# Optimization experiments

Measured on AMD Instinct MI355X. Metric: run time of the kernel, lower is better.

The kernel has to match this reference:

```python
import jax, jax.numpy as jnp
import numpy as np

B, T, C = 2, 2048, 1024
NH = 16
HD = C // NH

def setup_inputs() -> dict:
    key = jax.random.key(0)
    k1, k2, k3 = jax.random.split(key, 3)
    x = jax.random.normal(k1, (B, T, C), dtype=jnp.float32)
    w_attn = jax.random.normal(k2, (C, 3 * C), dtype=jnp.float32) * 0.02
    w_proj = jax.random.normal(k3, (C, C), dtype=jnp.float32) * 0.02
    return {"x": x, "w_attn": w_attn, "w_proj": w_proj}

def reference(x, w_attn, w_proj):
    b, t, c = x.shape
    qkv = x @ w_attn                                  # [B,T,3C]
    q, k, v = jnp.split(qkv, 3, axis=-1)
    # [B,NH,T,HD]
    q = q.reshape(b, t, NH, HD).transpose(0, 2, 1, 3)
    k = k.reshape(b, t, NH, HD).transpose(0, 2, 1, 3)
    v = v.reshape(b, t, NH, HD).transpose(0, 2, 1, 3)
    scale = 1.0 / np.sqrt(HD).astype(np.float32)
    att = jnp.einsum('bhqd,bhkd->bhqk', q, k) * scale  # [B,NH,T,T]
    causal = jnp.tril(jnp.ones((t, t), dtype=bool))
    att = jnp.where(causal[None, None], att, jnp.float32(-jnp.inf))
    att = jax.nn.softmax(att, axis=-1)
    y = jnp.einsum('bhqk,bhkd->bhqd', att, v)          # [B,NH,T,HD]
    y = y.transpose(0, 2, 1, 3).reshape(b, t, c)
    return y @ w_proj
```

## Files before the change

### kernel.cpp

```cpp
#include <hip/hip_runtime.h>
#include <hip/hip_bf16.h>

#define BB 2
#define TT 2048
#define CCH 1024
#define NHH 16
#define HDD 64
#define M_TOK (BB*TT)
#define N_QKV (3*CCH)

typedef __attribute__((ext_vector_type(8))) short bf16x8;
typedef __attribute__((ext_vector_type(4))) float f32x4;
typedef unsigned short u16;
typedef unsigned int u32;

__device__ __forceinline__ u16 f2bf(float f) {
    union { float f; u32 u; } v; v.f = f;
    u32 u = v.u;
    u32 r = (u + 0x7FFFu + ((u >> 16) & 1u)) >> 16;
    return (u16)r;
}

__device__ __forceinline__ u32 pk_bf16(float a, float b) {
    u32 ua = __float_as_uint(a) + 0x8000u;
    u32 ub = __float_as_uint(b) + 0x8000u;
    return __builtin_amdgcn_perm(ub, ua, 0x07060302u);
}

__device__ __forceinline__ void async_copy16(const void* g, void* l) {
    __builtin_amdgcn_global_load_lds((__attribute__((address_space(1))) void*)g,
                                     (__attribute__((address_space(3))) void*)l,
                                     16, 0, 0);
}


__global__ __launch_bounds__(256) void cast_bf16_kernel(
    const float* __restrict__ src, u16* __restrict__ dst, int n4) {
    int i = blockIdx.x * 256 + threadIdx.x;
    if (i < n4) {
        float4 f = ((const float4*)src)[i];
        ushort4 o;
        o.x = f2bf(f.x); o.y = f2bf(f.y); o.z = f2bf(f.z); o.w = f2bf(f.w);
        ((ushort4*)dst)[i] = o;
    }
}

__global__ __launch_bounds__(256) void transpose_bf16_kernel(
    const float* __restrict__ src, u16* __restrict__ dst, int R, int Cn,
    int scale_rows, float sc) {
    __shared__ float tile[32][33];
    int c0 = blockIdx.x * 32, r0 = blockIdx.y * 32;
    int tx = threadIdx.x, ty = threadIdx.y;
#pragma unroll
    for (int i = ty; i < 32; i += 8)
        tile[i][tx] = src[(size_t)(r0 + i) * Cn + c0 + tx];
    __syncthreads();
#pragma unroll
    for (int i = ty; i < 32; i += 8) {
        float v = tile[tx][i];
        if (c0 + i < scale_rows) v *= sc;
        dst[(size_t)(c0 + i) * R + r0 + tx] = f2bf(v);
    }
}


template<int SWAP, int NJ>
__device__ __forceinline__ void gemm_kloop64(
    const u16* __restrict__ A, const u16* __restrict__ Bt, int K,
    int m0, int n0, int t, u16* __restrict__ As, u16* __restrict__ Bs,
    f32x4 (&acc)[4][4])
{
    int lane = t & 63, w = t >> 6;
    int mw = (w >> 1) * 64, nw = (w & 1) * (NJ * 16);
    int mr = lane & 15, quad = lane >> 4;
    int lr = lane >> 3;
    int cswz = (lane & 7) ^ lr;

    const u16* gA[4]; u16* lA[4];
#pragma unroll
    for (int p = 0; p < 4; ++p) {
        int grp = w * 4 + p;
        gA[p] = A + (size_t)(m0 + grp * 8 + lr) * K + cswz * 8;
        lA[p] = As + ((size_t)grp * 64 + lane) * 8;
    }
    const u16* gB[4]; u16* lB[4];
#pragma unroll
    for (int p = 0; p < NJ; ++p) {
        int grp = w * NJ + p;
        gB[p] = Bt + (size_t)(n0 + grp * 8 + lr) * K + cswz * 8;
        lB[p] = Bs + ((size_t)grp * 64 + lane) * 8;
    }

    int swm = mr & 7;
    for (int k0 = 0; k0 < K; k0 += 64) {
#pragma unroll
        for (int p = 0; p < 4; ++p) async_copy16(gA[p] + k0, lA[p]);
#pragma unroll
        for (int p = 0; p < NJ; ++p) async_copy16(gB[p] + k0, lB[p]);
        __syncthreads();
#pragma unroll
        for (int kk = 0; kk < 2; ++kk) {
            bf16x8 af[4], bfr[4];
#pragma unroll
            for (int i = 0; i < 4; ++i) {
                int r = mw + i * 16 + mr;
                af[i] = *(const bf16x8*)&As[r * 64 + (((kk * 4 + quad) ^ swm) << 3)];
            }
#pragma unroll
            for (int j = 0; j < NJ; ++j) {
                int r = nw + j * 16 + mr;
                bfr[j] = *(const bf16x8*)&Bs[r * 64 + (((kk * 4 + quad) ^ swm) << 3)];
            }
#pragma unroll
            for (int i = 0; i < 4; ++i)
#pragma unroll
                for (int j = 0; j < NJ; ++j) {
                    if (SWAP)
                        acc[i][j] = __builtin_amdgcn_mfma_f32_16x16x32_bf16(bfr[j], af[i], acc[i][j], 0, 0, 0);
                    else
                        acc[i][j] = __builtin_amdgcn_mfma_f32_16x16x32_bf16(af[i], bfr[j], acc[i][j], 0, 0, 0);
                }
        }
        __syncthreads();
    }
}


#define QKV_NK 16
#define QKV_AS_HALF 16384
#define QKV_BS_HALF 12288
#define QKV_SMEM_BYTES ((2*QKV_AS_HALF + 2*QKV_BS_HALF) * 2)

__global__ __launch_bounds__(512, 1) void qkv_gemm_kernel(
    const u16* __restrict__ A, const u16* __restrict__ Bt,
    u16* __restrict__ Qo, u16* __restrict__ Ko, u16* __restrict__ Vto)
{
    extern __shared__ __align__(16) u16 smem[];
    u16* AsB = smem;
    u16* BsB = smem + 2 * QKV_AS_HALF;
    int t = threadIdx.x;
    int lane = t & 63, w = t >> 6;
    int m0 = blockIdx.y * 256, n0 = blockIdx.x * 192;
    int mw = (w >> 1) * 64, nw = (w & 1) * 96;
    int mr = lane & 15, quad = lane >> 4, swm = mr & 7;

    f32x4 zero = {0.f, 0.f, 0.f, 0.f};
    f32x4 acc[4][6];
#pragma unroll
    for (int i = 0; i < 4; ++i)
#pragma unroll
        for (int j = 0; j < 6; ++j) acc[i][j] = zero;

    int lr = lane >> 3;
    int cswz = (lane & 7) ^ lr;
    const u16* gA[4]; int lAo[4];
#pragma unroll
    for (int p = 0; p < 4; ++p) {
        int grp = w * 4 + p;
        gA[p] = A + (size_t)(m0 + grp * 8 + lr) * CCH + cswz * 8;
        lAo[p] = (grp * 64 + lane) * 8;
    }
    const u16* gB[3]; int lBo[3];
#pragma unroll
    for (int p = 0; p < 3; ++p) {
        int grp = w * 3 + p;
        gB[p] = Bt + (size_t)(n0 + grp * 8 + lr) * CCH + cswz * 8;
        lBo[p] = (grp * 64 + lane) * 8;
    }

#define QKV_STAGE(K0, BUF) do {                                               \
    u16* dA_ = AsB + (BUF) * QKV_AS_HALF;                                     \
    u16* dB_ = BsB + (BUF) * QKV_BS_HALF;                                     \
    _Pragma("unroll") for (int p_ = 0; p_ < 4; ++p_)                          \
        async_copy16(gA[p_] + (K0), dA_ + lAo[p_]);                           \
    _Pragma("unroll") for (int p_ = 0; p_ < 3; ++p_)                          \
        async_copy16(gB[p_] + (K0), dB_ + lBo[p_]);                           \
  } while (0)

    QKV_STAGE(0, 0);
    QKV_STAGE(64, 1);

    for (int k = 0; k < QKV_NK; ++k) {
        int cur = k & 1;
        if (k == QKV_NK - 1) asm volatile("s_waitcnt vmcnt(0)" ::: "memory");
        else                 asm volatile("s_waitcnt vmcnt(7)" ::: "memory");
        __builtin_amdgcn_s_barrier();
        asm volatile("" ::: "memory");
        const u16* Ac = AsB + cur * QKV_AS_HALF;
        const u16* Bc = BsB + cur * QKV_BS_HALF;
        bf16x8 a0[4], a1[4], b0[6], b1[6];
#pragma unroll
        for (int i = 0; i < 4; ++i) {
            int r = (mw + i * 16 + mr) * 64;
            a0[i] = *(const bf16x8*)&Ac[r + ((quad ^ swm) << 3)];
            a1[i] = *(const bf16x8*)&Ac[r + (((quad + 4) ^ swm) << 3)];
        }
#pragma unroll
        for (int j = 0; j < 6; ++j) {
            int r = (nw + j * 16 + mr) * 64;
            b0[j] = *(const bf16x8*)&Bc[r + ((quad ^ swm) << 3)];
            b1[j] = *(const bf16x8*)&Bc[r + (((quad + 4) ^ swm) << 3)];
        }
#pragma unroll
        for (int i = 0; i < 4; ++i)
#pragma unroll
            for (int j = 0; j < 6; ++j)
                acc[i][j] = __builtin_amdgcn_mfma_f32_16x16x32_bf16(b0[j], a0[i], acc[i][j], 0, 0, 0);
        asm volatile("s_waitcnt lgkmcnt(0)" ::: "memory");
        __builtin_amdgcn_sched_barrier(0);
        __builtin_amdgcn_s_barrier();
        asm volatile("" ::: "memory");
        if (k < QKV_NK - 2) QKV_STAGE((k + 2) * 64, cur);
#pragma unroll
        for (int i = 0; i < 4; ++i)
#pragma unroll
            for (int j = 0; j < 6; ++j)
                acc[i][j] = __builtin_amdgcn_mfma_f32_16x16x32_bf16(b1[j], a1[i], acc[i][j], 0, 0, 0);
    }
#undef QKV_STAGE

#pragma unroll
    for (int i = 0; i < 4; ++i)
#pragma unroll
        for (int j = 0; j < 6; ++j) {
            int tok = m0 + mw + i * 16 + mr;
            int cg0 = n0 + nw + j * 16 + quad * 4;
            int part = cg0 >> 10;
            int cc = cg0 & 1023;
            int h = cc >> 6, d0 = cc & 63;
            int b = tok >> 11, tt = tok & 2047;
            int bh = b * NHH + h;
            if (part < 2) {
                u16* dstp = part ? Ko : Qo;
                uint2 o;
                o.x = pk_bf16(acc[i][j][0], acc[i][j][1]);
                o.y = pk_bf16(acc[i][j][2], acc[i][j][3]);
                *(uint2*)&dstp[((size_t)bh * TT + tt) * HDD + d0] = o;
            } else {
#pragma unroll
                for (int r = 0; r < 4; ++r)
                    Vto[((size_t)bh * HDD + d0 + r) * TT + tt] = f2bf(acc[i][j][r]);
            }
        }
}


__global__ __launch_bounds__(256) void proj_gemm_kernel(
    const u16* __restrict__ A, const u16* __restrict__ Bt, float* __restrict__ Cout)
{
    __shared__ u16 As[128 * 64];
    __shared__ u16 Bs[64 * 64];
    int t = threadIdx.x;
    int m0 = blockIdx.y * 128, n0 = blockIdx.x * 64;
    int lane = t & 63, w = t >> 6;
    int mw = (w >> 1) * 64, nw = (w & 1) * 32;
    int mr = lane & 15, quad = lane >> 4;

    f32x4 zero = {0.f, 0.f, 0.f, 0.f};
    f32x4 acc[4][4];
#pragma unroll
    for (int i = 0; i < 4; ++i)
#pragma unroll
        for (int j = 0; j < 4; ++j) acc[i][j] = zero;

    gemm_kloop64<1, 2>(A, Bt, CCH, m0, n0, t, As, Bs, acc);

#pragma unroll
    for (int i = 0; i < 4; ++i)
#pragma unroll
        for (int j = 0; j < 2; ++j) {
            int tok = m0 + mw + i * 16 + mr;
            int cg0 = n0 + nw + j * 16 + quad * 4;
            float4 v;
            v.x = acc[i][j][0]; v.y = acc[i][j][1];
            v.z = acc[i][j][2]; v.w = acc[i][j][3];
            *(float4*)&Cout[(size_t)tok * CCH + cg0] = v;
        }
}


#define PST2 40

template<bool MASK>
__device__ __forceinline__ void tile3(
    const u16* __restrict__ Kb, const u16* __restrict__ Vb, u16* __restrict__ pb,
    bf16x8 qf0, bf16x8 qf1, bf16x8 ones, int m, int quad, int sw, int kh,
    int kvb, int qcol, f32x4 (&o)[4], f32x4& lacc)
{
    f32x4 zero = {0.f, 0.f, 0.f, 0.f};
#pragma unroll
    for (int kc = 0; kc < 2; ++kc) {
        int rr = kh * 32 + kc * 16 + m;
        bf16x8 kf0 = *(const bf16x8*)&Kb[rr * 64 + ((quad ^ sw) << 3)];
        bf16x8 kf1 = *(const bf16x8*)&Kb[rr * 64 + (((quad + 4) ^ sw) << 3)];
        f32x4 s  = __builtin_amdgcn_mfma_f32_16x16x32_bf16(kf0, qf0, zero, 0, 0, 0);
        f32x4 st = __builtin_amdgcn_mfma_f32_16x16x32_bf16(kf1, qf1, s, 0, 0, 0);
        float e0, e1, e2, e3;
#pragma unroll
        for (int r = 0; r < 4; ++r) {
            float v = st[r];
            if (MASK && (kvb + kc * 16 + quad * 4 + r > qcol)) v = -1e30f;
            float e = __builtin_amdgcn_exp2f(v);
            if (r == 0) e0 = e; else if (r == 1) e1 = e; else if (r == 2) e2 = e; else e3 = e;
        }
        uint2 pk; pk.x = pk_bf16(e0, e1); pk.y = pk_bf16(e2, e3);
        *(uint2*)&pb[m * PST2 + kc * 16 + quad * 4] = pk;
    }
    bf16x8 pf = *(const bf16x8*)&pb[m * PST2 + quad * 8];
    lacc = __builtin_amdgcn_mfma_f32_16x16x32_bf16(ones, pf, lacc, 0, 0, 0);
#pragma unroll
    for (int dg = 0; dg < 4; ++dg) {
        int rr = dg * 16 + m;
        bf16x8 vf = *(const bf16x8*)&Vb[rr * 64 + (((kh * 4 + quad) ^ sw) << 3)];
        o[dg] = __builtin_amdgcn_mfma_f32_16x16x32_bf16(vf, pf, o[dg], 0, 0, 0);
    }
}

#define SM_U16 26880

__global__ __launch_bounds__(512, 2) void attn_kernel(
    const u16* __restrict__ Q, const u16* __restrict__ K,
    const u16* __restrict__ Vt, u16* __restrict__ Y)
{
    __shared__ __align__(16) u16 smem[SM_U16];
    int t = threadIdx.x;
    int w = t >> 6, lane = t & 63;
    int m = lane & 15, quad = lane >> 4;
    int iq = w >> 1, kh = w & 1;

    int bid = blockIdx.x;
    int head = bid & 31;
    int g = bid >> 5;
    int pr = (g < 8) ? g : 23 - g;
    int qbA = pr;
    int qbB = 31 - pr;
    int rbA = qbA * 64 + iq * 16;
    int rbB = qbB * 64 + iq * 16;

    const u16* qpA = Q + ((size_t)head * TT + rbA + m) * HDD + quad * 8;
    const u16* qpB = Q + ((size_t)head * TT + rbB + m) * HDD + quad * 8;
    bf16x8 qA0 = *(const bf16x8*)qpA;
    bf16x8 qA1 = *(const bf16x8*)(qpA + 32);
    bf16x8 qB0 = *(const bf16x8*)qpB;
    bf16x8 qB1 = *(const bf16x8*)(qpB + 32);

    bf16x8 ones;
#pragma unroll
    for (int i = 0; i < 8; ++i) ones[i] = (short)0x3F80;

    const u16* kbase = K + (size_t)head * TT * HDD;
    const u16* vbase = Vt + (size_t)head * HDD * TT;
    u16* pbA = smem + 16384 + (w * 2 + 0) * (16 * PST2);
    u16* pbB = smem + 16384 + (w * 2 + 1) * (16 * PST2);

    int lr = lane >> 3;
    int cg = (lane & 7) ^ lr;
    int r0 = w * 8 + lr;
    int loff = (w * 64 + lane) * 8;

    f32x4 zero = {0.f, 0.f, 0.f, 0.f};
    f32x4 oA[4], oB[4], laA = zero, laB = zero;
#pragma unroll
    for (int dg = 0; dg < 4; ++dg) { oA[dg] = zero; oB[dg] = zero; }
    int qcA = rbA + m, qcB = rbB + m;
    int sw = m & 7;

    async_copy16(kbase + (size_t)r0 * 64 + cg * 8, smem + loff);
    async_copy16(vbase + (size_t)r0 * TT + cg * 8, smem + 8192 + loff);

    for (int ic = 0; ic <= qbB; ++ic) {
        int buf = ic & 1;
        int kv0 = ic << 6;
        __syncthreads();
        if (ic < qbB) {
            int nkv = kv0 + 64;
            u16* dK = smem + (buf ^ 1) * 4096;
            u16* dV = smem + 8192 + (buf ^ 1) * 4096;
            async_copy16(kbase + (size_t)(nkv + r0) * 64 + cg * 8, dK + loff);
            async_copy16(vbase + (size_t)r0 * TT + nkv + cg * 8, dV + loff);
        }
        const u16* Kb = smem + buf * 4096;
        const u16* Vb = smem + 8192 + buf * 4096;
        int kvb = kv0 + kh * 32;
        if (ic < qbA)
            tile3<false>(Kb, Vb, pbA, qA0, qA1, ones, m, quad, sw, kh, kvb, qcA, oA, laA);
        else if (ic == qbA)
            tile3<true >(Kb, Vb, pbA, qA0, qA1, ones, m, quad, sw, kh, kvb, qcA, oA, laA);
        if (ic < qbB)
            tile3<false>(Kb, Vb, pbB, qB0, qB1, ones, m, quad, sw, kh, kvb, qcB, oB, laB);
        else
            tile3<true >(Kb, Vb, pbB, qB0, qB1, ones, m, quad, sw, kh, kvb, qcB, oB, laB);
    }

    float lA = laA[0];
    float lB = laB[0];

    __syncthreads();
    f32x4* ob = (f32x4*)smem;
    float* lb = (float*)&smem[26624];
    if (kh) {
        f32x4* dst = ob + (size_t)iq * 512 + lane;
#pragma unroll
        for (int dg = 0; dg < 4; ++dg) {
            dst[dg * 64] = oA[dg];
            dst[(4 + dg) * 64] = oB[dg];
        }
        if (quad == 0) {
            lb[(iq * 2 + 0) * 16 + m] = lA;
            lb[(iq * 2 + 1) * 16 + m] = lB;
        }
    }
    __syncthreads();
    if (!kh) {
        f32x4* src = ob + (size_t)iq * 512 + lane;
#pragma unroll
        for (int dg = 0; dg < 4; ++dg) {
            oA[dg] += src[dg * 64];
            oB[dg] += src[(4 + dg) * 64];
        }
        lA += lb[(iq * 2 + 0) * 16 + m];
        lB += lb[(iq * 2 + 1) * 16 + m];
        float invA = 1.0f / lA, invB = 1.0f / lB;

        int b = head >> 4, h = head & 15;
        size_t roA = ((size_t)(b * TT + rbA + m)) * CCH + h * HDD;
        size_t roB = ((size_t)(b * TT + rbB + m)) * CCH + h * HDD;
#pragma unroll
        for (int dg = 0; dg < 4; ++dg) {
            uint2 ov;
            ov.x = pk_bf16(oA[dg][0] * invA, oA[dg][1] * invA);
            ov.y = pk_bf16(oA[dg][2] * invA, oA[dg][3] * invA);
            *(uint2*)&Y[roA + dg * 16 + quad * 4] = ov;
            ov.x = pk_bf16(oB[dg][0] * invB, oB[dg][1] * invB);
            ov.y = pk_bf16(oB[dg][2] * invB, oB[dg][3] * invB);
            *(uint2*)&Y[roB + dg * 16 + quad * 4] = ov;
        }
    }
}


extern "C" void kernel_launch(void* const* d_in, const int* in_sizes, int n_in,
                              void* d_out, int out_size, void* d_ws, size_t ws_size,
                              hipStream_t stream) {
    const float* x      = (const float*)d_in[0];
    const float* w_attn = (const float*)d_in[1];
    const float* w_proj = (const float*)d_in[2];
    float* out = (float*)d_out;

    char* ws = (char*)d_ws;
    u16* x_bf   = (u16*)ws; ws += (size_t)M_TOK * CCH * 2;
    u16* wqkvT  = (u16*)ws; ws += (size_t)N_QKV * CCH * 2;
    u16* wprojT = (u16*)ws; ws += (size_t)CCH * CCH * 2;
    u16* qbuf   = (u16*)ws; ws += (size_t)BB * NHH * TT * HDD * 2;
    u16* kbuf   = (u16*)ws; ws += (size_t)BB * NHH * TT * HDD * 2;
    u16* vtb    = (u16*)ws; ws += (size_t)BB * NHH * HDD * TT * 2;
    u16* yb     = (u16*)ws; ws += (size_t)M_TOK * CCH * 2;

    static bool attr_done = false;
    if (!attr_done) {
        (void)hipFuncSetAttribute(reinterpret_cast<const void*>(qkv_gemm_kernel),
                                  hipFuncAttributeMaxDynamicSharedMemorySize,
                                  QKV_SMEM_BYTES);
        attr_done = true;
    }

    const float QSC = 0.125f * 1.44269504088896f;

    cast_bf16_kernel<<<dim3(M_TOK * CCH / 4 / 256), dim3(256), 0, stream>>>(x, x_bf, M_TOK * CCH / 4);
    transpose_bf16_kernel<<<dim3(N_QKV / 32, CCH / 32), dim3(32, 8), 0, stream>>>(
        w_attn, wqkvT, CCH, N_QKV, CCH, QSC);
    transpose_bf16_kernel<<<dim3(CCH / 32, CCH / 32), dim3(32, 8), 0, stream>>>(
        w_proj, wprojT, CCH, CCH, 0, 1.0f);
    qkv_gemm_kernel<<<dim3(16, 16), dim3(512), QKV_SMEM_BYTES, stream>>>(
        x_bf, wqkvT, qbuf, kbuf, vtb);
    attn_kernel<<<dim3(512), dim3(512), 0, stream>>>(qbuf, kbuf, vtb, yb);
    proj_gemm_kernel<<<dim3(16, 32), dim3(256), 0, stream>>>(yb, wprojT, out);
}
```

Baseline: 166.0 us.

## Double-buffer proj GEMM with async prefetch and 128x128 tiles on 512 threads

Rewrites the output projection GEMM as a 512-thread block with 128x128 tiles. It uses two shared-memory buffers with async global-to-LDS prefetch two stages ahead, plus explicit waitcnt and barrier placement. This replaces the single-buffered shared gemm_kloop64, whose loads and MFMAs were separated by syncs every iteration, so load latency was exposed. The grid shrinks to 256 blocks with one block per CU, which may reduce latency hiding from occupancy.

```diff
diff --git a/kernel.cpp b/kernel.cpp
--- a/kernel.cpp
+++ b/kernel.cpp
@@ -60,68 +60,6 @@
         float v = tile[tx][i];
         if (c0 + i < scale_rows) v *= sc;
         dst[(size_t)(c0 + i) * R + r0 + tx] = f2bf(v);
-    }
-}
-
-
-template<int SWAP, int NJ>
-__device__ __forceinline__ void gemm_kloop64(
-    const u16* __restrict__ A, const u16* __restrict__ Bt, int K,
-    int m0, int n0, int t, u16* __restrict__ As, u16* __restrict__ Bs,
-    f32x4 (&acc)[4][4])
-{
-    int lane = t & 63, w = t >> 6;
-    int mw = (w >> 1) * 64, nw = (w & 1) * (NJ * 16);
-    int mr = lane & 15, quad = lane >> 4;
-    int lr = lane >> 3;
-    int cswz = (lane & 7) ^ lr;
-
-    const u16* gA[4]; u16* lA[4];
-#pragma unroll
-    for (int p = 0; p < 4; ++p) {
-        int grp = w * 4 + p;
-        gA[p] = A + (size_t)(m0 + grp * 8 + lr) * K + cswz * 8;
-        lA[p] = As + ((size_t)grp * 64 + lane) * 8;
-    }
-    const u16* gB[4]; u16* lB[4];
-#pragma unroll
-    for (int p = 0; p < NJ; ++p) {
-        int grp = w * NJ + p;
-        gB[p] = Bt + (size_t)(n0 + grp * 8 + lr) * K + cswz * 8;
-        lB[p] = Bs + ((size_t)grp * 64 + lane) * 8;
-    }
-
-    int swm = mr & 7;
-    for (int k0 = 0; k0 < K; k0 += 64) {
-#pragma unroll
-        for (int p = 0; p < 4; ++p) async_copy16(gA[p] + k0, lA[p]);
-#pragma unroll
-        for (int p = 0; p < NJ; ++p) async_copy16(gB[p] + k0, lB[p]);
-        __syncthreads();
-#pragma unroll
-        for (int kk = 0; kk < 2; ++kk) {
-            bf16x8 af[4], bfr[4];
-#pragma unroll
-            for (int i = 0; i < 4; ++i) {
-                int r = mw + i * 16 + mr;
-                af[i] = *(const bf16x8*)&As[r * 64 + (((kk * 4 + quad) ^ swm) << 3)];
-            }
-#pragma unroll
-            for (int j = 0; j < NJ; ++j) {
-                int r = nw + j * 16 + mr;
-                bfr[j] = *(const bf16x8*)&Bs[r * 64 + (((kk * 4 + quad) ^ swm) << 3)];
-            }
-#pragma unroll
-            for (int i = 0; i < 4; ++i)
-#pragma unroll
-                for (int j = 0; j < NJ; ++j) {
-                    if (SWAP)
-                        acc[i][j] = __builtin_amdgcn_mfma_f32_16x16x32_bf16(bfr[j], af[i], acc[i][j], 0, 0, 0);
-                    else
-                        acc[i][j] = __builtin_amdgcn_mfma_f32_16x16x32_bf16(af[i], bfr[j], acc[i][j], 0, 0, 0);
-                }
-        }
-        __syncthreads();
     }
 }
 
@@ -245,30 +183,101 @@
 }
 
 
-__global__ __launch_bounds__(256) void proj_gemm_kernel(
+#define PRJ_NK 16
+#define PRJ_AS_HALF 8192
+#define PRJ_SMEM_BYTES (4 * PRJ_AS_HALF * 2)
+
+__global__ __launch_bounds__(512, 1) void proj_gemm_kernel(
     const u16* __restrict__ A, const u16* __restrict__ Bt, float* __restrict__ Cout)
 {
-    __shared__ u16 As[128 * 64];
-    __shared__ u16 Bs[64 * 64];
+    extern __shared__ __align__(16) u16 psmem[];
+    u16* AsB = psmem;
+    u16* BsB = psmem + 2 * PRJ_AS_HALF;
     int t = threadIdx.x;
-    int m0 = blockIdx.y * 128, n0 = blockIdx.x * 64;
     int lane = t & 63, w = t >> 6;
-    int mw = (w >> 1) * 64, nw = (w & 1) * 32;
-    int mr = lane & 15, quad = lane >> 4;
+    int m0 = blockIdx.y * 128, n0 = blockIdx.x * 128;
+    int mw = (w >> 1) * 32, nw = (w & 1) * 64;
+    int mr = lane & 15, quad = lane >> 4, swm = mr & 7;
 
     f32x4 zero = {0.f, 0.f, 0.f, 0.f};
-    f32x4 acc[4][4];
-#pragma unroll
-    for (int i = 0; i < 4; ++i)
+    f32x4 acc[2][4];
+#pragma unroll
+    for (int i = 0; i < 2; ++i)
 #pragma unroll
         for (int j = 0; j < 4; ++j) acc[i][j] = zero;
 
-    gemm_kloop64<1, 2>(A, Bt, CCH, m0, n0, t, As, Bs, acc);
-
-#pragma unroll
-    for (int i = 0; i < 4; ++i)
-#pragma unroll
-        for (int j = 0; j < 2; ++j) {
+    int lr = lane >> 3;
+    int cswz = (lane & 7) ^ lr;
+    const u16* gA[2]; int lAo[2];
+#pragma unroll
+    for (int p = 0; p < 2; ++p) {
+        int grp = w * 2 + p;
+        gA[p] = A + (size_t)(m0 + grp * 8 + lr) * CCH + cswz * 8;
+        lAo[p] = (grp * 64 + lane) * 8;
+    }
+    const u16* gB[2]; int lBo[2];
+#pragma unroll
+    for (int p = 0; p < 2; ++p) {
+        int grp = w * 2 + p;
+        gB[p] = Bt + (size_t)(n0 + grp * 8 + lr) * CCH + cswz * 8;
+        lBo[p] = (grp * 64 + lane) * 8;
+    }
+
+#define PRJ_STAGE(K0, BUF) do {                                               \
+    u16* dA_ = AsB + (BUF) * PRJ_AS_HALF;                                     \
+    u16* dB_ = BsB + (BUF) * PRJ_AS_HALF;                                     \
+    _Pragma("unroll") for (int p_ = 0; p_ < 2; ++p_)                          \
+        async_copy16(gA[p_] + (K0), dA_ + lAo[p_]);                           \
+    _Pragma("unroll") for (int p_ = 0; p_ < 2; ++p_)                          \
+        async_copy16(gB[p_] + (K0), dB_ + lBo[p_]);                           \
+  } while (0)
+
+    PRJ_STAGE(0, 0);
+    PRJ_STAGE(64, 1);
+
+    for (int k = 0; k < PRJ_NK; ++k) {
+        int cur = k & 1;
+        if (k == PRJ_NK - 1) asm volatile("s_waitcnt vmcnt(0)" ::: "memory");
+        else                 asm volatile("s_waitcnt vmcnt(4)" ::: "memory");
+        __builtin_amdgcn_s_barrier();
+        asm volatile("" ::: "memory");
+        const u16* Ac = AsB + cur * PRJ_AS_HALF;
+        const u16* Bc = BsB + cur * PRJ_AS_HALF;
+        bf16x8 a0[2], a1[2], b0[4], b1[4];
+#pragma unroll
+        for (int i = 0; i < 2; ++i) {
+            int r = (mw + i * 16 + mr) * 64;
+            a0[i] = *(const bf16x8*)&Ac[r + ((quad ^ swm) << 3)];
+            a1[i] = *(const bf16x8*)&Ac[r + (((quad + 4) ^ swm) << 3)];
+        }
+#pragma unroll
+        for (int j = 0; j < 4; ++j) {
+            int r = (nw + j * 16 + mr) * 64;
+            b0[j] = *(const bf16x8*)&Bc[r + ((quad ^ swm) << 3)];
+            b1[j] = *(const bf16x8*)&Bc[r + (((quad + 4) ^ swm) << 3)];
+        }
+#pragma unroll
+        for (int i = 0; i < 2; ++i)
+#pragma unroll
+            for (int j = 0; j < 4; ++j)
+                acc[i][j] = __builtin_amdgcn_mfma_f32_16x16x32_bf16(b0[j], a0[i], acc[i][j], 0, 0, 0);
+        asm volatile("s_waitcnt lgkmcnt(0)" ::: "memory");
+        __builtin_amdgcn_sched_barrier(0);
+        __builtin_amdgcn_s_barrier();
+        asm volatile("" ::: "memory");
+        if (k < PRJ_NK - 2) PRJ_STAGE((k + 2) * 64, cur);
+#pragma unroll
+        for (int i = 0; i < 2; ++i)
+#pragma unroll
+            for (int j = 0; j < 4; ++j)
+                acc[i][j] = __builtin_amdgcn_mfma_f32_16x16x32_bf16(b1[j], a1[i], acc[i][j], 0, 0, 0);
+    }
+#undef PRJ_STAGE
+
+#pragma unroll
+    for (int i = 0; i < 2; ++i)
+#pragma unroll
+        for (int j = 0; j < 4; ++j) {
             int tok = m0 + mw + i * 16 + mr;
             int cg0 = n0 + nw + j * 16 + quad * 4;
             float4 v;
@@ -461,6 +470,9 @@
         (void)hipFuncSetAttribute(reinterpret_cast<const void*>(qkv_gemm_kernel),
                                   hipFuncAttributeMaxDynamicSharedMemorySize,
                                   QKV_SMEM_BYTES);
+        (void)hipFuncSetAttribute(reinterpret_cast<const void*>(proj_gemm_kernel),
+                                  hipFuncAttributeMaxDynamicSharedMemorySize,
+                                  PRJ_SMEM_BYTES);
         attr_done = true;
     }
 
@@ -474,5 +486,6 @@
     qkv_gemm_kernel<<<dim3(16, 16), dim3(512), QKV_SMEM_BYTES, stream>>>(
         x_bf, wqkvT, qbuf, kbuf, vtb);
     attn_kernel<<<dim3(512), dim3(512), 0, stream>>>(qbuf, kbuf, vtb, yb);
-    proj_gemm_kernel<<<dim3(16, 32), dim3(256), 0, stream>>>(yb, wprojT, out);
-}
+    proj_gemm_kernel<<<dim3(8, 32), dim3(512), PRJ_SMEM_BYTES, stream>>>(
+        yb, wprojT, out);
+}
```

New measurement: 162.9 us. About the same (-1.9%).
